# Kernel tuning notes

Measured on AMD Instinct MI355X. Metric: run time of the kernel, lower is better.

## Reference

```python
import jax
import jax.numpy as jnp
import numpy as np
from jax import lax

EPS = 0.1
MAX_ITER = 50
LOG_EPS = 1e-8


def _l2_normalize(a):
    # matches torch.nn.functional.normalize(p=2, dim=1) with eps=1e-12
    n = jnp.linalg.norm(a, axis=1, keepdims=True)
    return a / jnp.maximum(n, 1e-12)


def setup_inputs() -> dict:
    key = jax.random.key(0)
    k1, k2, k3 = jax.random.split(key, 3)
    B, K, D = 65536, 256, 128
    return {
        "x": jax.random.normal(k1, (B, D), dtype=jnp.float32),
        "prototypes": jax.random.normal(k2, (K, D), dtype=jnp.float32),
        "coordinates": jax.random.normal(k3, (B, K), dtype=jnp.float32),
    }


def reference(x, prototypes, coordinates):
    B = x.shape[0]
    K = prototypes.shape[0]
    # cosine cost matrix C: (B, K)
    xn = _l2_normalize(x)
    yn = _l2_normalize(prototypes)
    C = 1.0 - xn @ yn.T
    K_mat = jnp.exp(-C / EPS)
    logK = jnp.log(K_mat + LOG_EPS)  # (B, K)
    log_mu = jnp.log(1.0 / B + LOG_EPS)  # scalar (uniform marginals)
    log_nu = jnp.log(1.0 / K + LOG_EPS)

    def step(carry, _):
        u, v = carry
        u = log_mu - jax.scipy.special.logsumexp(logK + v[None, :], axis=1)
        v = log_nu - jax.scipy.special.logsumexp(logK + u[:, None], axis=0)
        return (u, v), None

    (u, v), _ = lax.scan(
        step,
        (jnp.zeros((B,), dtype=x.dtype), jnp.zeros((K,), dtype=x.dtype)),
        None,
        length=MAX_ITER,
    )
    pi = jnp.exp(u[:, None] + logK + v[None, :])  # (B, K) transport plan
    coord_weights = jax.nn.softmax(jnp.abs(coordinates), axis=1)
    return (pi * C * coord_weights).sum()
```

## Files before the change

kernel.cpp:

```cpp
#include <hip/hip_runtime.h>
#include <hip/hip_fp16.h>

#define B_N 65536
#define K_N 256
#define D_N 128
#define N_ITER 50
#define NSHARD 16
#define NBLK 256
#define GRPSZ 16
#define BUFSTRIDE (NSHARD * K_N)
#define EVPAD 20

#define BAR_LINES 65
#define BAR_ITER_U (BAR_LINES * 16)

constexpr float MU_EPS = 1.0f / 65536.0f + 1e-8f;
constexpr float NU_EPS = 1.0f / 256.0f + 1e-8f;
constexpr float KSCALE = 8192.0f;
constexpr float INV_KSCALE = 1.0f / 8192.0f;
constexpr float NUKS = NU_EPS * KSCALE;
constexpr float MUKS = MU_EPS * KSCALE;

typedef __attribute__((ext_vector_type(8))) short bf16x8;
typedef __attribute__((ext_vector_type(4))) float f32x4;

union frag_u { uint4 u; bf16x8 v; };

__device__ __forceinline__ float wave_sum(float v) {
#pragma unroll
    for (int m = 1; m < 64; m <<= 1) v += __shfl_xor(v, m, 64);
    return v;
}

__device__ __forceinline__ short f32_to_bf16(float x) {
    unsigned u = __float_as_uint(x);
    return (short)((u + 0x7FFFu + ((u >> 16) & 1u)) >> 16);
}
__device__ __forceinline__ float bf16_hi_f32(float x) {
    unsigned u = __float_as_uint(x);
    unsigned r = ((u + 0x7FFFu + ((u >> 16) & 1u)) >> 16) << 16;
    return __uint_as_float(r);
}

__global__ __launch_bounds__(64) void proto_norm_init(
        const float* __restrict__ proto, short* __restrict__ bh_s,
        short* __restrict__ bl_s, float* __restrict__ csbuf,
        unsigned* __restrict__ bar, float* __restrict__ out) {
    const int blk = blockIdx.x;
    const int lane = threadIdx.x;
    if (blk < 256) {
        float2 p = *(const float2*)&proto[blk * 128 + lane * 2];
        float ss = wave_sum(p.x * p.x + p.y * p.y);
        float inv = 1.0f / fmaxf(sqrtf(ss), 1e-12f);
        float v0 = p.x * inv, v1 = p.y * inv;
        short2 h, l;
        h.x = f32_to_bf16(v0); h.y = f32_to_bf16(v1);
        l.x = f32_to_bf16(v0 - bf16_hi_f32(v0));
        l.y = f32_to_bf16(v1 - bf16_hi_f32(v1));
        const int k0 = lane * 2;
        const int ks = k0 >> 5, qq = (k0 >> 3) & 3, j = k0 & 7;
        const int mm = blk & 15, CT = blk >> 4;
        const size_t off = (size_t)(((CT * 4 + ks) * 64 + qq * 16 + mm)) * 8 + j;
        *(short2*)&bh_s[off] = h;
        *(short2*)&bl_s[off] = l;
    } else {
        const int z = blk - 256;
        uint4* b4 = (uint4*)bar;
        const uint4 zero4 = {0u, 0u, 0u, 0u};
        const int total4 = N_ITER * BAR_ITER_U / 4;
        for (int i = z * 64 + lane; i < total4; i += 512) b4[i] = zero4;
        if (z == 0) {
            for (int i = lane; i < 3 * BUFSTRIDE; i += 64)
                csbuf[i] = (i >= 2 * BUFSTRIDE && i < 2 * BUFSTRIDE + K_N) ? NUKS : 0.0f;
            if (lane == 0) out[0] = 0.0f;
        }
    }
}

__global__ __launch_bounds__(1024, 4) void sinkhorn_persist(
        const float* __restrict__ x, const short* __restrict__ bh_s,
        const short* __restrict__ bl_s, float* __restrict__ csbuf,
        const float* __restrict__ coord, unsigned* __restrict__ bar,
        float* __restrict__ out) {
    __shared__ __align__(16) float ev_lds[16 * EVPAD];
    __shared__ float cs_lds[16 * 273];
    __shared__ float wpart[16];
    const int blk = blockIdx.x, tid = threadIdx.x;
    const int w = tid >> 6, lane = tid & 63;
    const int q = lane >> 4, m = lane & 15;

    const int arow = blk * 256 + w * 16 + m;
    float av[4][8];
    float ss = 0.0f;
#pragma unroll
    for (int ks = 0; ks < 4; ks++) {
        const float* ap = &x[(size_t)arow * 128 + ks * 32 + q * 8];
        float4 a0 = *(const float4*)ap;
        float4 a1 = *(const float4*)(ap + 4);
        av[ks][0] = a0.x; av[ks][1] = a0.y; av[ks][2] = a0.z; av[ks][3] = a0.w;
        av[ks][4] = a1.x; av[ks][5] = a1.y; av[ks][6] = a1.z; av[ks][7] = a1.w;
#pragma unroll
        for (int j = 0; j < 8; j++) ss = fmaf(av[ks][j], av[ks][j], ss);
    }
    ss += __shfl_xor(ss, 16, 64);
    ss += __shfl_xor(ss, 32, 64);
    const float rnv = 1.0f / fmaxf(sqrtf(ss), 1e-12f);
    frag_u ah[4], al[4];
#pragma unroll
    for (int ks = 0; ks < 4; ks++) {
        unsigned uh[4], ul[4];
#pragma unroll
        for (int p = 0; p < 4; p++) {
            float a0 = av[ks][2 * p] * rnv;
            float a1 = av[ks][2 * p + 1] * rnv;
            unsigned u;
            asm("v_cvt_pk_bf16_f32 %0, %1, %2" : "=v"(u) : "v"(a0), "v"(a1));
            float h0 = __uint_as_float(u << 16);
            float h1 = __uint_as_float(u & 0xffff0000u);
            float l0 = a0 - h0, l1 = a1 - h1;
            unsigned u2;
            asm("v_cvt_pk_bf16_f32 %0, %1, %2" : "=v"(u2) : "v"(l0), "v"(l1));
            uh[p] = u; ul[p] = u2;
        }
        ah[ks].u = make_uint4(uh[0], uh[1], uh[2], uh[3]);
        al[ks].u = make_uint4(ul[0], ul[1], ul[2], ul[3]);
    }
    float kvf[4][16];
    {
        f32x4 acc[16];
#pragma unroll
        for (int CT = 0; CT < 16; CT++) acc[CT] = (f32x4){0.f, 0.f, 0.f, 0.f};
#pragma unroll
        for (int ks = 0; ks < 4; ks++) {
#pragma unroll
            for (int CT = 0; CT < 16; CT++) {
                const size_t off = (size_t)(((CT * 4 + ks) * 64 + lane)) * 8;
                bf16x8 bh = *(const bf16x8*)&bh_s[off];
                bf16x8 bl = *(const bf16x8*)&bl_s[off];
                acc[CT] = __builtin_amdgcn_mfma_f32_16x16x32_bf16(ah[ks].v, bh, acc[CT], 0, 0, 0);
                acc[CT] = __builtin_amdgcn_mfma_f32_16x16x32_bf16(al[ks].v, bh, acc[CT], 0, 0, 0);
                acc[CT] = __builtin_amdgcn_mfma_f32_16x16x32_bf16(ah[ks].v, bl, acc[CT], 0, 0, 0);
            }
        }
#pragma unroll
        for (int CT = 0; CT < 16; CT++) {
#pragma unroll
            for (int r = 0; r < 4; r++) {
                float Cv = 1.0f - acc[CT][r];
                kvf[r][CT] = KSCALE * (__expf(-10.0f * Cv) + 1e-8f);
            }
        }
    }

    float ai_reg[4] = {0.f, 0.f, 0.f, 0.f};
    bool dead = false;
    for (int t = 0; t < N_ITER; t++) {
        const int p_read = (t + 2) % 3, p_acc = t % 3, p_zero = (t + 1) % 3;
        if (tid < 256) {
            const float* cb = csbuf + p_read * BUFSTRIDE;
            float cs = 0.0f;
#pragma unroll
            for (int s = 0; s < NSHARD; s++)
                cs += __hip_atomic_load(&cb[s * 256 + tid], __ATOMIC_RELAXED,
                                        __HIP_MEMORY_SCOPE_AGENT);
            ev_lds[(tid >> 4) * EVPAD + (tid & 15)] = NUKS * __builtin_amdgcn_rcpf(cs);
        }
        if (blk < NSHARD && tid < 256)
            __hip_atomic_store(&csbuf[p_zero * BUFSTRIDE + blk * 256 + tid], 0.0f,
                               __ATOMIC_RELAXED, __HIP_MEMORY_SCOPE_AGENT);
        __syncthreads();
        float e[16];
#pragma unroll
        for (int j = 0; j < 16; j++) e[j] = ev_lds[j * EVPAD + m];
        float acc[16];
#pragma unroll
        for (int j = 0; j < 16; j++) acc[j] = 0.0f;
#pragma unroll
        for (int rg = 0; rg < 4; rg++) {
            float part = 0.0f;
#pragma unroll
            for (int j = 0; j < 16; j++) part = fmaf(kvf[rg][j], e[j], part);
            part += __shfl_xor(part, 8, 64);
            part += __shfl_xor(part, 4, 64);
            part += __shfl_xor(part, 2, 64);
            part += __shfl_xor(part, 1, 64);
            float ai = MUKS * __builtin_amdgcn_rcpf(part);
            ai_reg[rg] = ai;
#pragma unroll
            for (int j = 0; j < 16; j++) acc[j] = fmaf(kvf[rg][j], ai, acc[j]);
        }
#pragma unroll
        for (int j = 0; j < 16; j++) {
            acc[j] += __shfl_xor(acc[j], 16, 64);
            acc[j] += __shfl_xor(acc[j], 32, 64);
        }
        if (q == 0) {
#pragma unroll
            for (int j = 0; j < 16; j++) cs_lds[w * 273 + j * 17 + m] = acc[j];
        }
        __syncthreads();
        if (tid < 256) {
            float v = 0.0f;
#pragma unroll
            for (int p = 0; p < 16; p++) v += cs_lds[p * 273 + (tid >> 4) * 17 + (tid & 15)];
            atomicAdd(&csbuf[p_acc * BUFSTRIDE + (blk & (NSHARD - 1)) * 256 + tid], v);
        }
        __syncthreads();
        if (tid == 0) {
            unsigned prev = __hip_atomic_fetch_add(
                &bar[t * BAR_ITER_U + (blk >> 4) * 16], 1u,
                __ATOMIC_RELAXED, __HIP_MEMORY_SCOPE_AGENT);
            if (prev == (unsigned)(GRPSZ - 1))
                __hip_atomic_store(&bar[t * BAR_ITER_U + (33 + (blk >> 4)) * 16], 1u,
                                   __ATOMIC_RELAXED, __HIP_MEMORY_SCOPE_AGENT);
        }
        if (w == 0 && !dead) {
            unsigned* dp = &bar[t * BAR_ITER_U + (33 + (lane & 15)) * 16];
            long long t0 = __builtin_amdgcn_s_memrealtime();
            while (true) {
                unsigned v = __hip_atomic_load(dp, __ATOMIC_RELAXED,
                                               __HIP_MEMORY_SCOPE_AGENT);
                if (__all(v != 0u)) break;
                __builtin_amdgcn_s_sleep(4);
                if (__builtin_amdgcn_s_memrealtime() - t0 > (1LL << 22)) {
                    dead = true;
                    break;
                }
            }
        }
        __syncthreads();
    }

    if (tid < 256) {
        const float* cb = csbuf + ((N_ITER - 1) % 3) * BUFSTRIDE;
        float cs = 0.0f;
#pragma unroll
        for (int s = 0; s < NSHARD; s++)
            cs += __hip_atomic_load(&cb[s * 256 + tid], __ATOMIC_RELAXED,
                                    __HIP_MEMORY_SCOPE_AGENT);
        ev_lds[(tid >> 4) * EVPAD + (tid & 15)] = NUKS * __builtin_amdgcn_rcpf(cs);
    }
    __syncthreads();
    float ef[16];
#pragma unroll
    for (int j = 0; j < 16; j++) ef[j] = ev_lds[j * EVPAD + m];
    float accv = 0.0f;
#pragma unroll
    for (int rg = 0; rg < 4; rg++) {
        const int row = blk * 256 + w * 16 + q * 4 + rg;
        float a[16];
#pragma unroll
        for (int j = 0; j < 16; j++)
            a[j] = fabsf(coord[(size_t)row * 256 + j * 16 + m]);
        float mx = a[0];
#pragma unroll
        for (int j = 1; j < 16; j++) mx = fmaxf(mx, a[j]);
        mx = fmaxf(mx, __shfl_xor(mx, 8, 64));
        mx = fmaxf(mx, __shfl_xor(mx, 4, 64));
        mx = fmaxf(mx, __shfl_xor(mx, 2, 64));
        mx = fmaxf(mx, __shfl_xor(mx, 1, 64));
        float ex[16];
        float zs = 0.0f;
#pragma unroll
        for (int j = 0; j < 16; j++) { ex[j] = __expf(a[j] - mx); zs += ex[j]; }
        zs += __shfl_xor(zs, 8, 64);
        zs += __shfl_xor(zs, 4, 64);
        zs += __shfl_xor(zs, 2, 64);
        zs += __shfl_xor(zs, 1, 64);
        float s = 0.0f;
#pragma unroll
        for (int j = 0; j < 16; j++) {
            float Cj = -0.1f * __logf(kvf[rg][j] * INV_KSCALE - 1e-8f);
            s += kvf[rg][j] * ef[j] * Cj * ex[j];
        }
        accv = fmaf(s, ai_reg[rg] * INV_KSCALE * __builtin_amdgcn_rcpf(zs), accv);
    }
    accv = wave_sum(accv);
    if (lane == 0) wpart[w] = accv;
    __syncthreads();
    if (tid == 0) {
        float tot = 0.0f;
#pragma unroll
        for (int i = 0; i < 16; i++) tot += wpart[i];
        atomicAdd(out, tot);
    }
}

extern "C" void kernel_launch(void* const* d_in, const int* in_sizes, int n_in,
                              void* d_out, int out_size, void* d_ws, size_t ws_size,
                              hipStream_t stream) {
    const float* x = (const float*)d_in[0];
    const float* proto = (const float*)d_in[1];
    const float* coord = (const float*)d_in[2];
    float* out = (float*)d_out;
    char* ws = (char*)d_ws;
    short* bh_s = (short*)(ws + 33554432);
    short* bl_s = bh_s + 32768;
    unsigned* bar = (unsigned*)(ws + 33554432 + 131072 + 262144);
    float* csbuf = (float*)(ws + 33554432 + 131072 + 262144 + 262144);

    hipLaunchKernelGGL(proto_norm_init, dim3(264), dim3(64), 0, stream,
                       proto, bh_s, bl_s, csbuf, bar, out);
    hipLaunchKernelGGL(sinkhorn_persist, dim3(NBLK), dim3(1024), 0, stream,
                       x, bh_s, bl_s, csbuf, coord, bar, out);
}
```

Measured before the change: 406.4 us.

## Replace two-level counter barrier with flag-array barrier polled by vector loads

Replaces the per-iteration hierarchical barrier (group atomic counters plus group-done flags, with fresh memory per iteration) with a single reused array of 256 per-block monotonic epoch flags. Each block stores its iteration number, and wave 0 polls all flags using one uncached dwordx4 load per lane and a shorter sleep. This removes the fetch-add serialization and the two-hop signalling latency, and it shrinks the barrier area the init kernel must zero. In exchange, every block now polls all 256 flags on each check, which adds memory traffic while blocks wait.

```diff
diff --git a/kernel.cpp b/kernel.cpp
--- a/kernel.cpp
+++ b/kernel.cpp
@@ -7,12 +7,10 @@
 #define N_ITER 50
 #define NSHARD 16
 #define NBLK 256
-#define GRPSZ 16
 #define BUFSTRIDE (NSHARD * K_N)
 #define EVPAD 20
 
-#define BAR_LINES 65
-#define BAR_ITER_U (BAR_LINES * 16)
+#define BAR_U (64 * 16)
 
 constexpr float MU_EPS = 1.0f / 65536.0f + 1e-8f;
 constexpr float NU_EPS = 1.0f / 256.0f + 1e-8f;
@@ -23,6 +21,7 @@
 
 typedef __attribute__((ext_vector_type(8))) short bf16x8;
 typedef __attribute__((ext_vector_type(4))) float f32x4;
+typedef __attribute__((ext_vector_type(4))) unsigned u32x4;
 
 union frag_u { uint4 u; bf16x8 v; };
 
@@ -64,16 +63,10 @@
         *(short2*)&bh_s[off] = h;
         *(short2*)&bl_s[off] = l;
     } else {
-        const int z = blk - 256;
-        uint4* b4 = (uint4*)bar;
-        const uint4 zero4 = {0u, 0u, 0u, 0u};
-        const int total4 = N_ITER * BAR_ITER_U / 4;
-        for (int i = z * 64 + lane; i < total4; i += 512) b4[i] = zero4;
-        if (z == 0) {
-            for (int i = lane; i < 3 * BUFSTRIDE; i += 64)
-                csbuf[i] = (i >= 2 * BUFSTRIDE && i < 2 * BUFSTRIDE + K_N) ? NUKS : 0.0f;
-            if (lane == 0) out[0] = 0.0f;
-        }
+        for (int i = lane; i < BAR_U; i += 64) bar[i] = 0u;
+        for (int i = lane; i < 3 * BUFSTRIDE; i += 64)
+            csbuf[i] = (i >= 2 * BUFSTRIDE && i < 2 * BUFSTRIDE + K_N) ? NUKS : 0.0f;
+        if (lane == 0) out[0] = 0.0f;
     }
 }
 
@@ -206,22 +199,20 @@
             atomicAdd(&csbuf[p_acc * BUFSTRIDE + (blk & (NSHARD - 1)) * 256 + tid], v);
         }
         __syncthreads();
-        if (tid == 0) {
-            unsigned prev = __hip_atomic_fetch_add(
-                &bar[t * BAR_ITER_U + (blk >> 4) * 16], 1u,
-                __ATOMIC_RELAXED, __HIP_MEMORY_SCOPE_AGENT);
-            if (prev == (unsigned)(GRPSZ - 1))
-                __hip_atomic_store(&bar[t * BAR_ITER_U + (33 + (blk >> 4)) * 16], 1u,
-                                   __ATOMIC_RELAXED, __HIP_MEMORY_SCOPE_AGENT);
-        }
+        if (tid == 0)
+            __hip_atomic_store(&bar[(blk & 63) * 16 + (blk >> 6)], (unsigned)(t + 1),
+                               __ATOMIC_RELAXED, __HIP_MEMORY_SCOPE_AGENT);
         if (w == 0 && !dead) {
-            unsigned* dp = &bar[t * BAR_ITER_U + (33 + (lane & 15)) * 16];
+            const unsigned T = (unsigned)(t + 1);
+            const unsigned* ap = &bar[lane * 16];
             long long t0 = __builtin_amdgcn_s_memrealtime();
             while (true) {
-                unsigned v = __hip_atomic_load(dp, __ATOMIC_RELAXED,
-                                               __HIP_MEMORY_SCOPE_AGENT);
-                if (__all(v != 0u)) break;
-                __builtin_amdgcn_s_sleep(4);
+                u32x4 v;
+                asm volatile("global_load_dwordx4 %0, %1, off sc0 sc1\n\t"
+                             "s_waitcnt vmcnt(0)"
+                             : "=v"(v) : "v"(ap) : "memory");
+                if (__all(v.x >= T && v.y >= T && v.z >= T && v.w >= T)) break;
+                __builtin_amdgcn_s_sleep(2);
                 if (__builtin_amdgcn_s_memrealtime() - t0 > (1LL << 22)) {
                     dead = true;
                     break;
@@ -299,7 +290,7 @@
     unsigned* bar = (unsigned*)(ws + 33554432 + 131072 + 262144);
     float* csbuf = (float*)(ws + 33554432 + 131072 + 262144 + 262144);
 
-    hipLaunchKernelGGL(proto_norm_init, dim3(264), dim3(64), 0, stream,
+    hipLaunchKernelGGL(proto_norm_init, dim3(257), dim3(64), 0, stream,
                        proto, bh_s, bl_s, csbuf, bar, out);
     hipLaunchKernelGGL(sinkhorn_persist, dim3(NBLK), dim3(1024), 0, stream,
                        x, bh_s, bl_s, csbuf, coord, bar, out);
```

New measurement: 411.8 us. About the same (+1.3%).
